# Optimization experiments

Measured on AMD Instinct MI355X. Metric: run time of the kernel, lower is better.

The kernel has to match this reference:

```python
import jax, jax.numpy as jnp
import numpy as np

D = 1024  # dim_context


def setup_inputs() -> dict:
    key = jax.random.key(0)
    k1, k2, k3, k4, k5 = jax.random.split(key, 5)
    B, T = 32, 2048
    hidden = jax.random.normal(k1, (B, D), dtype=jnp.float32)
    encoder_outputs = jax.random.normal(k2, (B, T, D), dtype=jnp.float32)
    # nn.Linear(2D, D): weight [D, 2D], bias [D]
    lim = 1.0 / np.sqrt(2 * D)
    W = jax.random.uniform(k3, (D, 2 * D), minval=-lim, maxval=lim, dtype=jnp.float32)
    b = jax.random.uniform(k4, (D,), minval=-lim, maxval=lim, dtype=jnp.float32)
    stdv = 1.0 / np.sqrt(D)
    v = jax.random.uniform(k5, (D,), minval=-stdv, maxval=stdv, dtype=jnp.float32)
    return {"hidden": hidden, "encoder_outputs": encoder_outputs, "W": W, "b": b, "v": v}


def reference(hidden, encoder_outputs, W, b, v):
    # hidden: [B, D]; encoder_outputs: [B, T, D]
    B, T, Dm = encoder_outputs.shape
    h = jnp.broadcast_to(hidden[:, None, :], (B, T, Dm))      # repeat over T
    attn_inputs = jnp.concatenate([h, encoder_outputs], axis=2)  # [B, T, 2D]
    energy = jax.nn.relu(jnp.einsum('btk,dk->btd', attn_inputs, W) + b)  # [B, T, D]
    scores = jnp.einsum('btd,d->bt', energy, v)                # [B, T]
    # softmax over dim=1 (time axis), then unsqueeze(1)
    return jax.nn.softmax(scores, axis=1)[:, None, :]          # [B, 1, T]
```

## Files before the change

kernel.cpp:

```cpp
#include <hip/hip_runtime.h>
#include <cstdint>


#define GLOBAL_AS __attribute__((address_space(1)))
#define LDS_AS    __attribute__((address_space(3)))

typedef __bf16 bf16x8 __attribute__((ext_vector_type(8)));
typedef float  f32x4  __attribute__((ext_vector_type(4)));

__device__ __forceinline__ unsigned int f2bf(float x) {
    unsigned int u = __builtin_bit_cast(unsigned int, x);
    u += 0x7fffu + ((u >> 16) & 1u);
    return u >> 16;
}

__global__ __launch_bounds__(256) void k_convert_enc(const float4* __restrict__ in,
                                                     uint4* __restrict__ out) {
    size_t idx = (size_t)blockIdx.x * 256 + threadIdx.x;
    float4 f0 = in[idx * 2];
    float4 f1 = in[idx * 2 + 1];
    uint4 o;
    o.x = f2bf(f0.x) | (f2bf(f0.y) << 16);
    o.y = f2bf(f0.z) | (f2bf(f0.w) << 16);
    o.z = f2bf(f1.x) | (f2bf(f1.y) << 16);
    o.w = f2bf(f1.z) | (f2bf(f1.w) << 16);
    out[idx] = o;
}

__global__ __launch_bounds__(256) void k_convert_we(const float* __restrict__ W,
                                                    uint2* __restrict__ out) {
    int idx = blockIdx.x * 256 + threadIdx.x;
    int i = idx * 4;
    int n = i >> 10, k = i & 1023;
    const float4 f = *(const float4*)(W + (size_t)n * 2048 + 1024 + k);
    uint2 o;
    o.x = f2bf(f.x) | (f2bf(f.y) << 16);
    o.y = f2bf(f.z) | (f2bf(f.w) << 16);
    out[idx] = o;
}

__global__ __launch_bounds__(256) void k_hidden_proj(const float* __restrict__ hidden,
                                                     const float* __restrict__ W,
                                                     const float* __restrict__ bias,
                                                     float* __restrict__ u) {
    int b  = threadIdx.x & 31;
    int dd = threadIdx.x >> 5;
    int d  = blockIdx.x * 8 + dd;
    const float* wrow = W + (size_t)d * 2048;
    const float* hrow = hidden + b * 1024;
    float acc = 0.f;
    for (int k = 0; k < 1024; k += 4) {
        float4 w4 = *(const float4*)(wrow + k);
        float4 h4 = *(const float4*)(hrow + k);
        acc += w4.x * h4.x + w4.y * h4.y + w4.z * h4.z + w4.w * h4.w;
    }
    u[b * 1024 + d] = acc + bias[d];
}

__global__ __launch_bounds__(256) void k_gemm_score(
        const unsigned short* __restrict__ A,
        const unsigned short* __restrict__ Bw,
        const float* __restrict__ u,
        const float* __restrict__ v,
        float* __restrict__ scores) {
    constexpr int K = 1024, BM = 128, BN = 128, BK = 32;
    __shared__ __align__(16) unsigned short As[BM * BK];
    __shared__ __align__(16) unsigned short Bs[BN * BK];

    const int tid  = threadIdx.x;
    const int wave = tid >> 6;
    const int lane = tid & 63;
    const int nb = blockIdx.x;
    const int mb = blockIdx.y;
    const int wm = wave & 1;
    const int wn = wave >> 1;
    const int q  = lane >> 4;
    const int cl = lane & 15;

    f32x4 acc[4][4];
    #pragma unroll
    for (int i = 0; i < 4; i++)
        #pragma unroll
        for (int j = 0; j < 4; j++)
            acc[i][j] = (f32x4){0.f, 0.f, 0.f, 0.f};

    const int rl  = lane >> 2;
    const int clk = (lane & 3) * 8;
    const unsigned short* Abase = A  + (size_t)(mb * BM) * K;
    const unsigned short* Bbase = Bw + (size_t)(nb * BN) * K;

    for (int k0 = 0; k0 < K; k0 += BK) {
        #pragma unroll
        for (int c = 0; c < 2; c++) {
            const int chunk = wave * 2 + c;
            const int row   = chunk * 16 + rl;
            const unsigned short* ga = Abase + (size_t)row * K + k0 + clk;
            const unsigned short* gb = Bbase + (size_t)row * K + k0 + clk;
            __builtin_amdgcn_global_load_lds((GLOBAL_AS void*)(size_t)ga,
                                             (LDS_AS void*)(As + chunk * 512), 16, 0, 0);
            __builtin_amdgcn_global_load_lds((GLOBAL_AS void*)(size_t)gb,
                                             (LDS_AS void*)(Bs + chunk * 512), 16, 0, 0);
        }
        __syncthreads();

        bf16x8 a[4], b[4];
        #pragma unroll
        for (int i = 0; i < 4; i++)
            a[i] = *(const bf16x8*)(As + (wm * 64 + i * 16 + cl) * BK + q * 8);
        #pragma unroll
        for (int j = 0; j < 4; j++)
            b[j] = *(const bf16x8*)(Bs + (wn * 64 + j * 16 + cl) * BK + q * 8);
        #pragma unroll
        for (int i = 0; i < 4; i++)
            #pragma unroll
            for (int j = 0; j < 4; j++)
                acc[i][j] = __builtin_amdgcn_mfma_f32_16x16x32_bf16(a[i], b[j], acc[i][j], 0, 0, 0);
        __syncthreads();
    }

    const int bidx = mb >> 4;
    float vv[4], uu[4];
    #pragma unroll
    for (int j = 0; j < 4; j++) {
        int n = nb * BN + wn * 64 + j * 16 + cl;
        vv[j] = v[n];
        uu[j] = u[bidx * 1024 + n];
    }
    #pragma unroll
    for (int i = 0; i < 4; i++) {
        #pragma unroll
        for (int r = 0; r < 4; r++) {
            float s = 0.f;
            #pragma unroll
            for (int j = 0; j < 4; j++) {
                float e = acc[i][j][r] + uu[j];
                s += fmaxf(e, 0.f) * vv[j];
            }
            s += __shfl_xor(s, 1);
            s += __shfl_xor(s, 2);
            s += __shfl_xor(s, 4);
            s += __shfl_xor(s, 8);
            if (cl == 0) {
                int m = mb * BM + wm * 64 + i * 16 + q * 4 + r;
                atomicAdd(&scores[m], s);
            }
        }
    }
}

__global__ __launch_bounds__(256) void k_softmax(const float* __restrict__ scores,
                                                 float* __restrict__ out) {
    __shared__ float red[4];
    int b  = blockIdx.x;
    int t0 = threadIdx.x;
    int wave = threadIdx.x >> 6, lane = threadIdx.x & 63;
    const float* s = scores + b * 2048;
    float vals[8];
    float lmax = -1e30f;
    #pragma unroll
    for (int i = 0; i < 8; i++) {
        vals[i] = s[t0 + i * 256];
        lmax = fmaxf(lmax, vals[i]);
    }
    for (int o = 32; o > 0; o >>= 1) lmax = fmaxf(lmax, __shfl_xor(lmax, o));
    if (lane == 0) red[wave] = lmax;
    __syncthreads();
    float gmax = fmaxf(fmaxf(red[0], red[1]), fmaxf(red[2], red[3]));
    float lsum = 0.f;
    #pragma unroll
    for (int i = 0; i < 8; i++) {
        vals[i] = expf(vals[i] - gmax);
        lsum += vals[i];
    }
    for (int o = 32; o > 0; o >>= 1) lsum += __shfl_xor(lsum, o);
    __syncthreads();
    if (lane == 0) red[wave] = lsum;
    __syncthreads();
    float inv = 1.0f / (red[0] + red[1] + red[2] + red[3]);
    #pragma unroll
    for (int i = 0; i < 8; i++) out[b * 2048 + t0 + i * 256] = vals[i] * inv;
}

extern "C" void kernel_launch(void* const* d_in, const int* in_sizes, int n_in,
                              void* d_out, int out_size, void* d_ws, size_t ws_size,
                              hipStream_t stream) {
    const float* hidden = (const float*)d_in[0];
    const float* enc    = (const float*)d_in[1];
    const float* W      = (const float*)d_in[2];
    const float* bias   = (const float*)d_in[3];
    const float* v      = (const float*)d_in[4];
    float* out = (float*)d_out;

    char* ws = (char*)d_ws;
    unsigned short* encb = (unsigned short*)ws;
    unsigned short* Web  = (unsigned short*)(ws + 134217728);
    float* u      = (float*)(ws + 134217728 + 2097152);
    float* scores = (float*)(ws + 134217728 + 2097152 + 131072);

    hipMemsetAsync(scores, 0, 65536 * sizeof(float), stream);
    k_convert_enc<<<32768, 256, 0, stream>>>((const float4*)enc, (uint4*)encb);
    k_convert_we<<<1024, 256, 0, stream>>>(W, (uint2*)Web);
    k_hidden_proj<<<128, 256, 0, stream>>>(hidden, W, bias, u);
    dim3 g(8, 512);
    k_gemm_score<<<g, 256, 0, stream>>>(encb, Web, u, v, scores);
    k_softmax<<<32, 256, 0, stream>>>(scores, out);
}
```

Baseline: 619.0 us.

## Fuse encoder bf16 conversion into GEMM, loop N-tiles per block, swizzle LDS

The separate fp32-to-bf16 conversion pass over the encoder outputs is removed. Each GEMM block now owns one 128-row M tile and loops over all 8 N tiles. On the first N tile it converts the fp32 rows inline, writes them to LDS and to a bf16 workspace copy, and later N tiles reload that copy. Score partials accumulate in registers and are reduced through LDS, which removes the atomics and the memset. The patch also adds an XOR swizzle on the LDS fragments and rewrites hidden_proj to use one block per output column, at the cost of only 512 blocks and a serialized fp32 load on the first pass.

```diff
diff --git a/kernel.cpp b/kernel.cpp
--- a/kernel.cpp
+++ b/kernel.cpp
@@ -14,17 +14,13 @@
     return u >> 16;
 }
 
-__global__ __launch_bounds__(256) void k_convert_enc(const float4* __restrict__ in,
-                                                     uint4* __restrict__ out) {
-    size_t idx = (size_t)blockIdx.x * 256 + threadIdx.x;
-    float4 f0 = in[idx * 2];
-    float4 f1 = in[idx * 2 + 1];
+__device__ __forceinline__ uint4 pack8(float4 f0, float4 f1) {
     uint4 o;
     o.x = f2bf(f0.x) | (f2bf(f0.y) << 16);
     o.y = f2bf(f0.z) | (f2bf(f0.w) << 16);
     o.z = f2bf(f1.x) | (f2bf(f1.y) << 16);
     o.w = f2bf(f1.z) | (f2bf(f1.w) << 16);
-    out[idx] = o;
+    return o;
 }
 
 __global__ __launch_bounds__(256) void k_convert_we(const float* __restrict__ W,
@@ -43,115 +39,161 @@
                                                      const float* __restrict__ W,
                                                      const float* __restrict__ bias,
                                                      float* __restrict__ u) {
-    int b  = threadIdx.x & 31;
-    int dd = threadIdx.x >> 5;
-    int d  = blockIdx.x * 8 + dd;
-    const float* wrow = W + (size_t)d * 2048;
-    const float* hrow = hidden + b * 1024;
+    __shared__ float wrow[1024];
+    __shared__ float red[256];
+    const int tid = threadIdx.x, d = blockIdx.x;
+    ((float4*)wrow)[tid] = ((const float4*)(W + (size_t)d * 2048))[tid];
+    __syncthreads();
+    const int b = tid & 31, kc = tid >> 5;
+    const float* h = hidden + b * 1024 + kc * 128;
+    const float* w = wrow + kc * 128;
     float acc = 0.f;
-    for (int k = 0; k < 1024; k += 4) {
-        float4 w4 = *(const float4*)(wrow + k);
-        float4 h4 = *(const float4*)(hrow + k);
-        acc += w4.x * h4.x + w4.y * h4.y + w4.z * h4.z + w4.w * h4.w;
-    }
-    u[b * 1024 + d] = acc + bias[d];
+    #pragma unroll 8
+    for (int i = 0; i < 128; i += 4) {
+        float4 hv = *(const float4*)(h + i);
+        acc += w[i] * hv.x + w[i + 1] * hv.y + w[i + 2] * hv.z + w[i + 3] * hv.w;
+    }
+    red[tid] = acc;
+    __syncthreads();
+    if (tid < 32) {
+        float s = 0.f;
+        #pragma unroll
+        for (int j = 0; j < 8; j++) s += red[j * 32 + tid];
+        u[tid * 1024 + d] = s + bias[d];
+    }
 }
 
 __global__ __launch_bounds__(256) void k_gemm_score(
-        const unsigned short* __restrict__ A,
+        const float* __restrict__ Af,
+        unsigned short* __restrict__ Ab,
         const unsigned short* __restrict__ Bw,
         const float* __restrict__ u,
         const float* __restrict__ v,
         float* __restrict__ scores) {
-    constexpr int K = 1024, BM = 128, BN = 128, BK = 32;
-    __shared__ __align__(16) unsigned short As[BM * BK];
-    __shared__ __align__(16) unsigned short Bs[BN * BK];
+    constexpr int K = 1024, BK = 32;
+    __shared__ __align__(16) unsigned short As[128 * BK];
+    __shared__ __align__(16) unsigned short Bs[128 * BK];
+    __shared__ float red[2][128];
 
     const int tid  = threadIdx.x;
     const int wave = tid >> 6;
     const int lane = tid & 63;
-    const int nb = blockIdx.x;
-    const int mb = blockIdx.y;
-    const int wm = wave & 1;
-    const int wn = wave >> 1;
-    const int q  = lane >> 4;
-    const int cl = lane & 15;
-
+    const int mb   = blockIdx.x;
+    const int wm = wave & 1, wn = wave >> 1;
+    const int q = lane >> 4, cl = lane & 15;
+
+    int aoff[4], boff[4];
+    #pragma unroll
+    for (int i = 0; i < 4; i++) {
+        int ra = wm * 64 + i * 16 + cl;
+        aoff[i] = ra * BK + (q ^ ((ra >> 1) & 3)) * 8;
+        int rb = wn * 64 + i * 16 + cl;
+        boff[i] = rb * BK + (q ^ ((rb >> 1) & 3)) * 8;
+    }
+
+    const int rl  = lane >> 2;
+    const int kbs = lane & 3;
+    int srow[2], skb[2];
+    #pragma unroll
+    for (int c = 0; c < 2; c++) {
+        int chunk = wave * 2 + c;
+        srow[c] = chunk * 16 + rl;
+        skb[c]  = kbs ^ ((srow[c] >> 1) & 3);
+    }
+
+    float sacc[4][4];
+    #pragma unroll
+    for (int i = 0; i < 4; i++)
+        #pragma unroll
+        for (int r = 0; r < 4; r++) sacc[i][r] = 0.f;
+
+    const int bidx = mb >> 4;
     f32x4 acc[4][4];
+
+    for (int nb = 0; nb < 8; nb++) {
+        #pragma unroll
+        for (int i = 0; i < 4; i++)
+            #pragma unroll
+            for (int j = 0; j < 4; j++) acc[i][j] = (f32x4){0.f, 0.f, 0.f, 0.f};
+
+        for (int k0 = 0; k0 < K; k0 += BK) {
+            if (nb == 0) {
+                #pragma unroll
+                for (int c = 0; c < 2; c++) {
+                    const int chunk = wave * 2 + c;
+                    const size_t aidx = (size_t)(mb * 128 + srow[c]) * K + k0 + skb[c] * 8;
+                    const float4* gs = (const float4*)(Af + aidx);
+                    uint4 o = pack8(gs[0], gs[1]);
+                    *(uint4*)(As + chunk * 512 + lane * 8) = o;
+                    *(uint4*)(Ab + aidx) = o;
+                    const unsigned short* gb = Bw + (size_t)srow[c] * K + k0 + skb[c] * 8;
+                    __builtin_amdgcn_global_load_lds((GLOBAL_AS void*)(size_t)gb,
+                                                     (LDS_AS void*)(Bs + chunk * 512), 16, 0, 0);
+                }
+            } else {
+                #pragma unroll
+                for (int c = 0; c < 2; c++) {
+                    const int chunk = wave * 2 + c;
+                    const unsigned short* ga = Ab + (size_t)(mb * 128 + srow[c]) * K + k0 + skb[c] * 8;
+                    const unsigned short* gb = Bw + (size_t)(nb * 128 + srow[c]) * K + k0 + skb[c] * 8;
+                    __builtin_amdgcn_global_load_lds((GLOBAL_AS void*)(size_t)ga,
+                                                     (LDS_AS void*)(As + chunk * 512), 16, 0, 0);
+                    __builtin_amdgcn_global_load_lds((GLOBAL_AS void*)(size_t)gb,
+                                                     (LDS_AS void*)(Bs + chunk * 512), 16, 0, 0);
+                }
+            }
+            __syncthreads();
+            bf16x8 afr[4], bfr[4];
+            #pragma unroll
+            for (int i = 0; i < 4; i++) afr[i] = *(const bf16x8*)(As + aoff[i]);
+            #pragma unroll
+            for (int j = 0; j < 4; j++) bfr[j] = *(const bf16x8*)(Bs + boff[j]);
+            #pragma unroll
+            for (int i = 0; i < 4; i++)
+                #pragma unroll
+                for (int j = 0; j < 4; j++)
+                    acc[i][j] = __builtin_amdgcn_mfma_f32_16x16x32_bf16(afr[i], bfr[j], acc[i][j], 0, 0, 0);
+            __syncthreads();
+        }
+
+        float vv[4], uu[4];
+        #pragma unroll
+        for (int j = 0; j < 4; j++) {
+            int n = nb * 128 + wn * 64 + j * 16 + cl;
+            vv[j] = v[n];
+            uu[j] = u[bidx * 1024 + n];
+        }
+        #pragma unroll
+        for (int i = 0; i < 4; i++)
+            #pragma unroll
+            for (int r = 0; r < 4; r++) {
+                float s = sacc[i][r];
+                #pragma unroll
+                for (int j = 0; j < 4; j++)
+                    s += fmaxf(acc[i][j][r] + uu[j], 0.f) * vv[j];
+                sacc[i][r] = s;
+            }
+    }
+
     #pragma unroll
     for (int i = 0; i < 4; i++)
         #pragma unroll
-        for (int j = 0; j < 4; j++)
-            acc[i][j] = (f32x4){0.f, 0.f, 0.f, 0.f};
-
-    const int rl  = lane >> 2;
-    const int clk = (lane & 3) * 8;
-    const unsigned short* Abase = A  + (size_t)(mb * BM) * K;
-    const unsigned short* Bbase = Bw + (size_t)(nb * BN) * K;
-
-    for (int k0 = 0; k0 < K; k0 += BK) {
-        #pragma unroll
-        for (int c = 0; c < 2; c++) {
-            const int chunk = wave * 2 + c;
-            const int row   = chunk * 16 + rl;
-            const unsigned short* ga = Abase + (size_t)row * K + k0 + clk;
-            const unsigned short* gb = Bbase + (size_t)row * K + k0 + clk;
-            __builtin_amdgcn_global_load_lds((GLOBAL_AS void*)(size_t)ga,
-                                             (LDS_AS void*)(As + chunk * 512), 16, 0, 0);
-            __builtin_amdgcn_global_load_lds((GLOBAL_AS void*)(size_t)gb,
-                                             (LDS_AS void*)(Bs + chunk * 512), 16, 0, 0);
-        }
-        __syncthreads();
-
-        bf16x8 a[4], b[4];
-        #pragma unroll
-        for (int i = 0; i < 4; i++)
-            a[i] = *(const bf16x8*)(As + (wm * 64 + i * 16 + cl) * BK + q * 8);
-        #pragma unroll
-        for (int j = 0; j < 4; j++)
-            b[j] = *(const bf16x8*)(Bs + (wn * 64 + j * 16 + cl) * BK + q * 8);
-        #pragma unroll
-        for (int i = 0; i < 4; i++)
-            #pragma unroll
-            for (int j = 0; j < 4; j++)
-                acc[i][j] = __builtin_amdgcn_mfma_f32_16x16x32_bf16(a[i], b[j], acc[i][j], 0, 0, 0);
-        __syncthreads();
-    }
-
-    const int bidx = mb >> 4;
-    float vv[4], uu[4];
-    #pragma unroll
-    for (int j = 0; j < 4; j++) {
-        int n = nb * BN + wn * 64 + j * 16 + cl;
-        vv[j] = v[n];
-        uu[j] = u[bidx * 1024 + n];
-    }
-    #pragma unroll
-    for (int i = 0; i < 4; i++) {
-        #pragma unroll
         for (int r = 0; r < 4; r++) {
-            float s = 0.f;
-            #pragma unroll
-            for (int j = 0; j < 4; j++) {
-                float e = acc[i][j][r] + uu[j];
-                s += fmaxf(e, 0.f) * vv[j];
-            }
+            float s = sacc[i][r];
             s += __shfl_xor(s, 1);
             s += __shfl_xor(s, 2);
             s += __shfl_xor(s, 4);
             s += __shfl_xor(s, 8);
-            if (cl == 0) {
-                int m = mb * BM + wm * 64 + i * 16 + q * 4 + r;
-                atomicAdd(&scores[m], s);
-            }
+            if (cl == 0) red[wn][wm * 64 + i * 16 + q * 4 + r] = s;
         }
-    }
+    __syncthreads();
+    if (tid < 128) scores[mb * 128 + tid] = red[0][tid] + red[1][tid];
 }
 
 __global__ __launch_bounds__(256) void k_softmax(const float* __restrict__ scores,
                                                  float* __restrict__ out) {
     __shared__ float red[4];
-    int b  = blockIdx.x;
+    int b = blockIdx.x;
     int t0 = threadIdx.x;
     int wave = threadIdx.x >> 6, lane = threadIdx.x & 63;
     const float* s = scores + b * 2048;
@@ -197,11 +239,8 @@
     float* u      = (float*)(ws + 134217728 + 2097152);
     float* scores = (float*)(ws + 134217728 + 2097152 + 131072);
 
-    hipMemsetAsync(scores, 0, 65536 * sizeof(float), stream);
-    k_convert_enc<<<32768, 256, 0, stream>>>((const float4*)enc, (uint4*)encb);
+    k_hidden_proj<<<1024, 256, 0, stream>>>(hidden, W, bias, u);
     k_convert_we<<<1024, 256, 0, stream>>>(W, (uint2*)Web);
-    k_hidden_proj<<<128, 256, 0, stream>>>(hidden, W, bias, u);
-    dim3 g(8, 512);
-    k_gemm_score<<<g, 256, 0, stream>>>(encb, Web, u, v, scores);
+    k_gemm_score<<<512, 256, 0, stream>>>(enc, encb, Web, u, v, scores);
     k_softmax<<<32, 256, 0, stream>>>(scores, out);
 }
```

After: 625.6 us. Within noise of the previous version (+1.1%).
